# Kernel optimization log

Hardware: AMD Instinct MI355X
Metric: run time of the kernel (lower is better)

Reference implementation:

```python
import jax, jax.numpy as jnp
import numpy as np

N_NODES = 100000
N_EDGES = 1600000
IN_DIM, HID_DIM, LAT_DIM = 128, 128, 32


def setup_inputs() -> dict:
    key = jax.random.key(0)
    k_x, k_e, k_w1, k_w2 = jax.random.split(key, 4)
    x = jax.random.normal(k_x, (N_NODES, IN_DIM), dtype=jnp.float32)
    edge_index = jax.random.randint(k_e, (2, N_EDGES), 0, N_NODES, dtype=jnp.int64)
    # GCNConv weights (glorot-ish scale) and biases
    W1 = jax.random.normal(k_w1, (IN_DIM, HID_DIM), dtype=jnp.float32) / np.sqrt(IN_DIM)
    b1 = jnp.zeros((HID_DIM,), dtype=jnp.float32)
    W2 = jax.random.normal(k_w2, (HID_DIM, LAT_DIM), dtype=jnp.float32) / np.sqrt(HID_DIM)
    b2 = jnp.zeros((LAT_DIM,), dtype=jnp.float32)
    return {"x": x, "edge_index": edge_index, "W1": W1, "b1": b1, "W2": W2, "b2": b2}


def _gcn_layer(x, W, b, src, dst, deg_inv_sqrt, n_nodes):
    # x: [N, Din] -> [N, Dout]; PyG GCNConv: transform, normalize, scatter-add
    xw = x @ W  # [N, Dout]
    norm = deg_inv_sqrt[src] * deg_inv_sqrt[dst]  # [E+N] (self-loops included)
    msg = xw[src] * norm[:, None]  # gather + scale  [E+N, Dout]
    out = jax.ops.segment_sum(msg, dst, num_segments=n_nodes)
    return out + b


def reference(x, edge_index, W1, b1, W2, b2):
    n = x.shape[0]
    loops = jnp.arange(n, dtype=edge_index.dtype)
    # add self-loops (GCNConv default)
    src = jnp.concatenate([edge_index[0], loops])
    dst = jnp.concatenate([edge_index[1], loops])
    # symmetric normalization: deg computed on destination (incl. self-loops)
    deg = jax.ops.segment_sum(jnp.ones_like(dst, dtype=x.dtype), dst, num_segments=n)
    deg_inv_sqrt = jnp.where(deg > 0, jax.lax.rsqrt(deg), 0.0)

    h = _gcn_layer(x, W1, b1, src, dst, deg_inv_sqrt, n)
    h = jax.nn.relu(h)
    # dropout is identity in eval mode
    z = _gcn_layer(h, W2, b2, src, dst, deg_inv_sqrt, n)
    return z
```

## Files before the change

kernel.cpp:

```cpp
#include <hip/hip_runtime.h>


#define KDIM 128
#define PA_NB 196
#define PA_CAP 64
#define PB_CAP 10240

typedef unsigned int uint;
typedef unsigned short ushort;
typedef __attribute__((ext_vector_type(8))) short bf16x8;
typedef __attribute__((ext_vector_type(4))) float f32x4;

__device__ inline ushort f2bf(float f) {
    uint u = __float_as_uint(f);
    return (ushort)((u + 0x7fffu + ((u >> 16) & 1u)) >> 16);
}

__global__ void initw_kernel(int* wcnt, int nwin) {
    int b = threadIdx.x;
    if (b < nwin) wcnt[b] = 0;
}

__global__ __launch_bounds__(256)
void wincount_kernel(const int* __restrict__ dst, int* __restrict__ wcnt, int e, int nwin) {
    __shared__ int lcnt[PA_NB];
    const int tid = threadIdx.x;
    for (int b = tid; b < nwin; b += 256) lcnt[b] = 0;
    __syncthreads();
    int i = blockIdx.x * blockDim.x + tid;
    const int stride = gridDim.x * blockDim.x;
    for (; i < e; i += stride) atomicAdd(&lcnt[dst[i] >> 9], 1);
    __syncthreads();
    for (int b = tid; b < nwin; b += 256) {
        int v = lcnt[b];
        if (v) atomicAdd(&wcnt[b], v);
    }
}

__global__ __launch_bounds__(256)
void winscan_kernel(const int* __restrict__ wcnt, int* __restrict__ winbase,
                    int* __restrict__ gcur, int nwin, int e) {
    __shared__ int ts[256];
    const int t = threadIdx.x;
    int v = (t < nwin) ? wcnt[t] : 0;
    ts[t] = v;
    for (int off = 1; off < 256; off <<= 1) {
        __syncthreads();
        int u = (t >= off) ? ts[t - off] : 0;
        __syncthreads();
        ts[t] += u;
    }
    __syncthreads();
    if (t < nwin) {
        int base = ts[t] - v;
        winbase[t] = base;
        gcur[t] = base;
    }
    if (t == 0) winbase[nwin] = e;
}

__global__ __launch_bounds__(256)
void binA_kernel(const int* __restrict__ src, const int* __restrict__ dst,
                 int* __restrict__ gcur, int* __restrict__ tmp, int e, int nb) {
    __shared__ int lbuf[PA_NB * PA_CAP];
    __shared__ int cnt[PA_NB];
    __shared__ int gbase[PA_NB];
    const int tid = threadIdx.x;
    for (int b = tid; b < nb; b += 256) cnt[b] = 0;
    __syncthreads();

    const int per = (e + gridDim.x - 1) / gridDim.x;
    const int i0 = blockIdx.x * per;
    const int i1 = min(i0 + per, e);
    for (int i = i0 + tid; i < i1; i += 256) {
        int d = dst[i];
        int s = src[i];
        int b = d >> 9;
        int rec = ((d & 511) << 17) | s;
        int p = atomicAdd(&cnt[b], 1);
        if (p < PA_CAP) lbuf[b * PA_CAP + p] = rec;
        else tmp[atomicAdd(&gcur[b], 1)] = rec;
    }
    __syncthreads();
    if (tid < nb) {
        int lvl = min(cnt[tid], PA_CAP);
        cnt[tid] = lvl;
        gbase[tid] = lvl ? atomicAdd(&gcur[tid], lvl) : 0;
    }
    __syncthreads();
    for (int bb = 0; bb < nb; bb += 4) {
        int b = bb + (tid >> 6);
        if (b < nb) {
            int lvl = cnt[b];
            int l = tid & 63;
            if (l < lvl) tmp[gbase[b] + l] = lbuf[b * PA_CAP + l];
        }
    }
}

__global__ __launch_bounds__(256)
void sortB_kernel(const int* __restrict__ tmp, const int* __restrict__ winbase,
                  int* __restrict__ offs, float* __restrict__ dinv,
                  int* __restrict__ csr, int n, int e) {
    __shared__ int lcsr[PB_CAP];
    __shared__ int cnt[512];
    __shared__ int ts[256];
    const int w = blockIdx.x;
    const int tid = threadIdx.x;
    const int node0 = w << 9;
    const int nloc = min(512, n - node0);
    const int base = winbase[w];
    const int end  = winbase[w + 1];

    for (int j = tid; j < 512; j += 256) cnt[j] = 0;
    __syncthreads();
    for (int i = base + tid; i < end; i += 256)
        atomicAdd(&cnt[(tmp[i] >> 17) & 511], 1);
    __syncthreads();

    int a0 = cnt[2 * tid], a1 = cnt[2 * tid + 1];
    int sum = a0 + a1;
    ts[tid] = sum;
    for (int off = 1; off < 256; off <<= 1) {
        __syncthreads();
        int v = (tid >= off) ? ts[tid - off] : 0;
        __syncthreads();
        ts[tid] += v;
    }
    __syncthreads();
    const int ex = ts[tid] - sum;
    if (2 * tid < nloc) {
        offs[node0 + 2 * tid] = base + ex;
        dinv[node0 + 2 * tid] = rsqrtf((float)(a0 + 1));
    }
    if (2 * tid + 1 < nloc) {
        offs[node0 + 2 * tid + 1] = base + ex + a0;
        dinv[node0 + 2 * tid + 1] = rsqrtf((float)(a1 + 1));
    }
    cnt[2 * tid] = ex;
    cnt[2 * tid + 1] = ex + a0;
    if (w == gridDim.x - 1 && tid == 0) offs[n] = e;
    __syncthreads();

    for (int i = base + tid; i < end; i += 256) {
        int rec = tmp[i];
        int dl = (rec >> 17) & 511;
        int s = rec & 0x1FFFF;
        int p = atomicAdd(&cnt[dl], 1);
        if (p < PB_CAP) lcsr[p] = s;
        else csr[base + p] = s;
    }
    __syncthreads();
    const int lim = min(end - base, PB_CAP);
    for (int i = tid; i < lim; i += 256) csr[base + i] = lcsr[i];
}

template<int DOUT>
__global__ void packW_kernel(const float* __restrict__ W, ushort* __restrict__ Wf) {
    int idx = blockIdx.x * blockDim.x + threadIdx.x;
    if (idx >= 128 * DOUT) return;
    int k = idx / DOUT, col = idx % DOUT;
    int c = col >> 4, lcol = col & 15;
    int t = k >> 5, u = (k >> 3) & 3, j = k & 7;
    int lane = u * 16 + lcol;
    Wf[(size_t)(((c * 4 + t) * 64 + lane) * 8 + j)] = f2bf(W[idx]);
}

__global__ __launch_bounds__(256)
void mfma1_kernel(const float* __restrict__ x, const ushort* __restrict__ W1f,
                  const float* __restrict__ dinv, ushort* __restrict__ outb, int n) {
    __shared__ ushort bsm[16384];
    const int tid = threadIdx.x;
    #pragma unroll
    for (int j = 0; j < 8; ++j)
        ((uint4*)bsm)[tid + j * 256] = ((const uint4*)W1f)[tid + j * 256];

    const int w = tid >> 6;
    const int lane = tid & 63;
    const int r = lane & 15;
    const int u = lane >> 4;
    const int row0 = blockIdx.x * 64 + w * 16;
    int arow = row0 + r; if (arow >= n) arow = n - 1;

    bf16x8 afr[4];
    #pragma unroll
    for (int t = 0; t < 4; ++t) {
        const float* px = &x[(size_t)arow * 128 + t * 32 + u * 8];
        f32x4 v0 = *(const f32x4*)px;
        f32x4 v1 = *(const f32x4*)(px + 4);
        bf16x8 a;
        a[0] = (short)f2bf(v0[0]); a[1] = (short)f2bf(v0[1]);
        a[2] = (short)f2bf(v0[2]); a[3] = (short)f2bf(v0[3]);
        a[4] = (short)f2bf(v1[0]); a[5] = (short)f2bf(v1[1]);
        a[6] = (short)f2bf(v1[2]); a[7] = (short)f2bf(v1[3]);
        afr[t] = a;
    }
    __syncthreads();

    f32x4 acc[8];
    #pragma unroll
    for (int c = 0; c < 8; ++c) acc[c] = (f32x4){0.f, 0.f, 0.f, 0.f};

    #pragma unroll
    for (int c = 0; c < 8; ++c) {
        #pragma unroll
        for (int t = 0; t < 4; ++t) {
            bf16x8 b = *(const bf16x8*)&bsm[(size_t)(((c * 4 + t) * 64 + lane) * 8)];
            acc[c] = __builtin_amdgcn_mfma_f32_16x16x32_bf16(afr[t], b, acc[c], 0, 0, 0);
        }
    }

    const int rb = row0 + u * 4;
    f32x4 d4 = *(const f32x4*)&dinv[(rb + 3 < n) ? rb : 0];
    #pragma unroll
    for (int c = 0; c < 8; ++c) {
        #pragma unroll
        for (int rr = 0; rr < 4; ++rr) {
            int row = rb + rr;
            if (row < n) outb[(size_t)row * 128 + c * 16 + r] = f2bf(acc[c][rr] * d4[rr]);
        }
    }
}

__global__ __launch_bounds__(256)
void mfma2_kernel(const ushort* __restrict__ hb, const ushort* __restrict__ W2f,
                  const float* __restrict__ dinv, ushort* __restrict__ outb, int n) {
    __shared__ ushort bsm[4096];
    const int tid = threadIdx.x;
    #pragma unroll
    for (int j = 0; j < 2; ++j)
        ((uint4*)bsm)[tid + j * 256] = ((const uint4*)W2f)[tid + j * 256];

    const int w = tid >> 6;
    const int lane = tid & 63;
    const int r = lane & 15;
    const int u = lane >> 4;
    const int row0 = blockIdx.x * 64 + w * 16;
    int arow = row0 + r; if (arow >= n) arow = n - 1;

    bf16x8 afr[4];
    #pragma unroll
    for (int t = 0; t < 4; ++t)
        afr[t] = *(const bf16x8*)&hb[(size_t)arow * 128 + t * 32 + u * 8];
    __syncthreads();

    f32x4 acc[2];
    acc[0] = (f32x4){0.f, 0.f, 0.f, 0.f};
    acc[1] = (f32x4){0.f, 0.f, 0.f, 0.f};
    #pragma unroll
    for (int c = 0; c < 2; ++c) {
        #pragma unroll
        for (int t = 0; t < 4; ++t) {
            bf16x8 b = *(const bf16x8*)&bsm[(size_t)(((c * 4 + t) * 64 + lane) * 8)];
            acc[c] = __builtin_amdgcn_mfma_f32_16x16x32_bf16(afr[t], b, acc[c], 0, 0, 0);
        }
    }

    const int rb = row0 + u * 4;
    f32x4 d4 = *(const f32x4*)&dinv[(rb + 3 < n) ? rb : 0];
    #pragma unroll
    for (int c = 0; c < 2; ++c) {
        #pragma unroll
        for (int rr = 0; rr < 4; ++rr) {
            int row = rb + rr;
            if (row < n) outb[(size_t)row * 32 + c * 16 + r] = f2bf(acc[c][rr] * d4[rr]);
        }
    }
}

__device__ inline void bf2_add(uint u, float& a0, float& a1) {
    a0 += __uint_as_float(u << 16);
    a1 += __uint_as_float(u & 0xffff0000u);
}

__device__ inline void bf8_add(uint4 u, float* acc) {
    bf2_add(u.x, acc[0], acc[1]);
    bf2_add(u.y, acc[2], acc[3]);
    bf2_add(u.z, acc[4], acc[5]);
    bf2_add(u.w, acc[6], acc[7]);
}

__global__ __launch_bounds__(256)
void agg128_kernel(const ushort* __restrict__ xwb, const int* __restrict__ offs,
                   const int* __restrict__ csr, const float* __restrict__ dinv,
                   const float* __restrict__ bias, ushort* __restrict__ outb, int n) {
    const int w = threadIdx.x >> 6;
    const int i = blockIdx.x * 4 + w;
    if (i >= n) return;
    const int lane = threadIdx.x & 63;
    const int g = lane >> 4;
    const int q = lane & 15;

    float acc[8] = {};
    const int e0 = offs[i], e1 = offs[i + 1];
    int e = e0 + g;
    for (; e + 12 < e1; e += 16) {
        int s0 = csr[e];
        int s1 = csr[e + 4];
        int s2 = csr[e + 8];
        int s3 = csr[e + 12];
        uint4 u0 = *(const uint4*)&xwb[(size_t)s0 * 128 + q * 8];
        uint4 u1 = *(const uint4*)&xwb[(size_t)s1 * 128 + q * 8];
        uint4 u2 = *(const uint4*)&xwb[(size_t)s2 * 128 + q * 8];
        uint4 u3 = *(const uint4*)&xwb[(size_t)s3 * 128 + q * 8];
        bf8_add(u0, acc);
        bf8_add(u1, acc);
        bf8_add(u2, acc);
        bf8_add(u3, acc);
    }
    for (; e < e1; e += 4) {
        int s0 = csr[e];
        uint4 u = *(const uint4*)&xwb[(size_t)s0 * 128 + q * 8];
        bf8_add(u, acc);
    }
    #pragma unroll
    for (int j = 0; j < 8; ++j) {
        acc[j] += __shfl_xor(acc[j], 16, 64);
        acc[j] += __shfl_xor(acc[j], 32, 64);
    }

    if (g == 0) {
        const float di = dinv[i];
        uint4 su = *(const uint4*)&xwb[(size_t)i * 128 + q * 8];
        bf8_add(su, acc);
        const float4 b0 = *(const float4*)&bias[q * 8];
        const float4 b1 = *(const float4*)&bias[q * 8 + 4];
        ushort us[8];
        us[0] = f2bf(fmaxf(acc[0] * di + b0.x, 0.f));
        us[1] = f2bf(fmaxf(acc[1] * di + b0.y, 0.f));
        us[2] = f2bf(fmaxf(acc[2] * di + b0.z, 0.f));
        us[3] = f2bf(fmaxf(acc[3] * di + b0.w, 0.f));
        us[4] = f2bf(fmaxf(acc[4] * di + b1.x, 0.f));
        us[5] = f2bf(fmaxf(acc[5] * di + b1.y, 0.f));
        us[6] = f2bf(fmaxf(acc[6] * di + b1.z, 0.f));
        us[7] = f2bf(fmaxf(acc[7] * di + b1.w, 0.f));
        *(uint4*)&outb[(size_t)i * 128 + q * 8] = *(const uint4*)us;
    }
}

__global__ __launch_bounds__(256)
void agg32_kernel(const ushort* __restrict__ xwb, const int* __restrict__ offs,
                  const int* __restrict__ csr, const float* __restrict__ dinv,
                  const float* __restrict__ bias, float* __restrict__ out, int n) {
    const int w = threadIdx.x >> 6;
    const int i = blockIdx.x * 4 + w;
    if (i >= n) return;
    const int lane = threadIdx.x & 63;
    const int g = lane >> 3;
    const int q = lane & 7;

    float acc[4] = {};
    const int e0 = offs[i], e1 = offs[i + 1];
    int e = e0 + g;
    for (; e + 8 < e1; e += 16) {
        int s0 = csr[e];
        int s1 = csr[e + 8];
        uint2 u0 = *(const uint2*)&xwb[(size_t)s0 * 32 + q * 4];
        uint2 u1 = *(const uint2*)&xwb[(size_t)s1 * 32 + q * 4];
        bf2_add(u0.x, acc[0], acc[1]);
        bf2_add(u0.y, acc[2], acc[3]);
        bf2_add(u1.x, acc[0], acc[1]);
        bf2_add(u1.y, acc[2], acc[3]);
    }
    if (e < e1) {
        int s0 = csr[e];
        uint2 u = *(const uint2*)&xwb[(size_t)s0 * 32 + q * 4];
        bf2_add(u.x, acc[0], acc[1]);
        bf2_add(u.y, acc[2], acc[3]);
    }
    #pragma unroll
    for (int j = 0; j < 4; ++j) {
        acc[j] += __shfl_xor(acc[j], 8, 64);
        acc[j] += __shfl_xor(acc[j], 16, 64);
        acc[j] += __shfl_xor(acc[j], 32, 64);
    }

    if (g == 0) {
        const float di = dinv[i];
        uint2 su = *(const uint2*)&xwb[(size_t)i * 32 + q * 4];
        bf2_add(su.x, acc[0], acc[1]);
        bf2_add(su.y, acc[2], acc[3]);
        const float4 b = *(const float4*)&bias[q * 4];
        float4 r;
        r.x = acc[0] * di + b.x;
        r.y = acc[1] * di + b.y;
        r.z = acc[2] * di + b.z;
        r.w = acc[3] * di + b.w;
        *(float4*)&out[(size_t)i * 32 + q * 4] = r;
    }
}

extern "C" void kernel_launch(void* const* d_in, const int* in_sizes, int n_in,
                              void* d_out, int out_size, void* d_ws, size_t ws_size,
                              hipStream_t stream) {
    const int n = in_sizes[0] / KDIM;
    const int e = in_sizes[1] / 2;

    const float* x  = (const float*)d_in[0];
    const int*   ei = (const int*)d_in[1];
    const int*   src = ei;
    const int*   dst = ei + e;
    const float* W1 = (const float*)d_in[2];
    const float* b1 = (const float*)d_in[3];
    const float* W2 = (const float*)d_in[4];
    const float* b2 = (const float*)d_in[5];
    float* out = (float*)d_out;

    char* p = (char*)d_ws;
    auto alloc = [&](size_t bytes) { char* q = p; p += (bytes + 255) & ~(size_t)255; return q; };
    const int nwin = (n + 511) >> 9;
    float*  dinv    = (float*)alloc((size_t)n * 4);
    int*    offs    = (int*)  alloc((size_t)(n + 1) * 4);
    int*    wcnt    = (int*)  alloc((size_t)nwin * 4);
    int*    winbase = (int*)  alloc((size_t)(nwin + 1) * 4);
    int*    gcur    = (int*)  alloc((size_t)nwin * 4);
    int*    csr     = (int*)  alloc((size_t)e * 4);
    ushort* W1f     = (ushort*)alloc((size_t)128 * 128 * 2);
    ushort* W2f     = (ushort*)alloc((size_t)128 * 32 * 2);
    ushort* xws1    = (ushort*)alloc((size_t)n * 128 * 2);
    ushort* hb      = (ushort*)alloc((size_t)n * 128 * 2);
    ushort* xw2s    = (ushort*)alloc((size_t)n * 32 * 2);
    int*    tmp     = (int*)hb;

    initw_kernel<<<1, 256, 0, stream>>>(wcnt, nwin);
    wincount_kernel<<<1024, 256, 0, stream>>>(dst, wcnt, e, nwin);
    winscan_kernel<<<1, 256, 0, stream>>>(wcnt, winbase, gcur, nwin, e);
    binA_kernel<<<512, 256, 0, stream>>>(src, dst, gcur, tmp, e, nwin);
    sortB_kernel<<<nwin, 256, 0, stream>>>(tmp, winbase, offs, dinv, csr, n, e);
    packW_kernel<128><<<64, 256, 0, stream>>>(W1, W1f);
    packW_kernel<32><<<16, 256, 0, stream>>>(W2, W2f);

    mfma1_kernel<<<(n + 63) / 64, 256, 0, stream>>>(x, W1f, dinv, xws1, n);
    agg128_kernel<<<(n + 3) / 4, 256, 0, stream>>>(xws1, offs, csr, dinv, b1, hb, n);

    mfma2_kernel<<<(n + 63) / 64, 256, 0, stream>>>(hb, W2f, dinv, xw2s, n);
    agg32_kernel<<<(n + 3) / 4, 256, 0, stream>>>(xw2s, offs, csr, dinv, b2, out, n);
}
```

Baseline: 209.1 us.

## Merge weight packing, memset counters, double rows per MFMA block, shrink agg unroll

```diff
diff --git a/kernel.cpp b/kernel.cpp
--- a/kernel.cpp
+++ b/kernel.cpp
@@ -14,11 +14,6 @@
 __device__ inline ushort f2bf(float f) {
     uint u = __float_as_uint(f);
     return (ushort)((u + 0x7fffu + ((u >> 16) & 1u)) >> 16);
-}
-
-__global__ void initw_kernel(int* wcnt, int nwin) {
-    int b = threadIdx.x;
-    if (b < nwin) wcnt[b] = 0;
 }
 
 __global__ __launch_bounds__(256)
@@ -155,15 +150,23 @@
     for (int i = tid; i < lim; i += 256) csr[base + i] = lcsr[i];
 }
 
-template<int DOUT>
-__global__ void packW_kernel(const float* __restrict__ W, ushort* __restrict__ Wf) {
+__global__ void packW_kernel(const float* __restrict__ W1, ushort* __restrict__ W1f,
+                             const float* __restrict__ W2, ushort* __restrict__ W2f) {
     int idx = blockIdx.x * blockDim.x + threadIdx.x;
-    if (idx >= 128 * DOUT) return;
-    int k = idx / DOUT, col = idx % DOUT;
-    int c = col >> 4, lcol = col & 15;
-    int t = k >> 5, u = (k >> 3) & 3, j = k & 7;
-    int lane = u * 16 + lcol;
-    Wf[(size_t)(((c * 4 + t) * 64 + lane) * 8 + j)] = f2bf(W[idx]);
+    if (idx < 16384) {
+        int k = idx >> 7, col = idx & 127;
+        int c = col >> 4, lcol = col & 15;
+        int t = k >> 5, u = (k >> 3) & 3, j = k & 7;
+        int lane = u * 16 + lcol;
+        W1f[(size_t)(((c * 4 + t) * 64 + lane) * 8 + j)] = f2bf(W1[idx]);
+    } else if (idx < 16384 + 4096) {
+        int i2 = idx - 16384;
+        int k = i2 >> 5, col = i2 & 31;
+        int c = col >> 4, lcol = col & 15;
+        int t = k >> 5, u = (k >> 3) & 3, j = k & 7;
+        int lane = u * 16 + lcol;
+        W2f[(size_t)(((c * 4 + t) * 64 + lane) * 8 + j)] = f2bf(W2[i2]);
+    }
 }
 
 __global__ __launch_bounds__(256)
@@ -174,50 +177,52 @@
     #pragma unroll
     for (int j = 0; j < 8; ++j)
         ((uint4*)bsm)[tid + j * 256] = ((const uint4*)W1f)[tid + j * 256];
+    __syncthreads();
 
     const int w = tid >> 6;
     const int lane = tid & 63;
     const int r = lane & 15;
     const int u = lane >> 4;
-    const int row0 = blockIdx.x * 64 + w * 16;
-    int arow = row0 + r; if (arow >= n) arow = n - 1;
-
-    bf16x8 afr[4];
-    #pragma unroll
-    for (int t = 0; t < 4; ++t) {
-        const float* px = &x[(size_t)arow * 128 + t * 32 + u * 8];
-        f32x4 v0 = *(const f32x4*)px;
-        f32x4 v1 = *(const f32x4*)(px + 4);
-        bf16x8 a;
-        a[0] = (short)f2bf(v0[0]); a[1] = (short)f2bf(v0[1]);
-        a[2] = (short)f2bf(v0[2]); a[3] = (short)f2bf(v0[3]);
-        a[4] = (short)f2bf(v1[0]); a[5] = (short)f2bf(v1[1]);
-        a[6] = (short)f2bf(v1[2]); a[7] = (short)f2bf(v1[3]);
-        afr[t] = a;
-    }
-    __syncthreads();
-
-    f32x4 acc[8];
-    #pragma unroll
-    for (int c = 0; c < 8; ++c) acc[c] = (f32x4){0.f, 0.f, 0.f, 0.f};
-
-    #pragma unroll
-    for (int c = 0; c < 8; ++c) {
+
+    for (int rt = 0; rt < 2; ++rt) {
+        const int row0 = blockIdx.x * 128 + rt * 64 + w * 16;
+        int arow = row0 + r; if (arow >= n) arow = n - 1;
+
+        bf16x8 afr[4];
         #pragma unroll
         for (int t = 0; t < 4; ++t) {
-            bf16x8 b = *(const bf16x8*)&bsm[(size_t)(((c * 4 + t) * 64 + lane) * 8)];
-            acc[c] = __builtin_amdgcn_mfma_f32_16x16x32_bf16(afr[t], b, acc[c], 0, 0, 0);
-        }
-    }
-
-    const int rb = row0 + u * 4;
-    f32x4 d4 = *(const f32x4*)&dinv[(rb + 3 < n) ? rb : 0];
-    #pragma unroll
-    for (int c = 0; c < 8; ++c) {
-        #pragma unroll
-        for (int rr = 0; rr < 4; ++rr) {
-            int row = rb + rr;
-            if (row < n) outb[(size_t)row * 128 + c * 16 + r] = f2bf(acc[c][rr] * d4[rr]);
+            const float* px = &x[(size_t)arow * 128 + t * 32 + u * 8];
+            f32x4 v0 = *(const f32x4*)px;
+            f32x4 v1 = *(const f32x4*)(px + 4);
+            bf16x8 a;
+            a[0] = (short)f2bf(v0[0]); a[1] = (short)f2bf(v0[1]);
+            a[2] = (short)f2bf(v0[2]); a[3] = (short)f2bf(v0[3]);
+            a[4] = (short)f2bf(v1[0]); a[5] = (short)f2bf(v1[1]);
+            a[6] = (short)f2bf(v1[2]); a[7] = (short)f2bf(v1[3]);
+            afr[t] = a;
+        }
+
+        f32x4 acc[8];
+        #pragma unroll
+        for (int c = 0; c < 8; ++c) acc[c] = (f32x4){0.f, 0.f, 0.f, 0.f};
+        #pragma unroll
+        for (int c = 0; c < 8; ++c) {
+            #pragma unroll
+            for (int t = 0; t < 4; ++t) {
+                bf16x8 b = *(const bf16x8*)&bsm[(size_t)(((c * 4 + t) * 64 + lane) * 8)];
+                acc[c] = __builtin_amdgcn_mfma_f32_16x16x32_bf16(afr[t], b, acc[c], 0, 0, 0);
+            }
+        }
+
+        const int rb = row0 + u * 4;
+        f32x4 d4 = *(const f32x4*)&dinv[(rb + 3 < n) ? rb : 0];
+        #pragma unroll
+        for (int c = 0; c < 8; ++c) {
+            #pragma unroll
+            for (int rr = 0; rr < 4; ++rr) {
+                int row = rb + rr;
+                if (row < n) outb[(size_t)row * 128 + c * 16 + r] = f2bf(acc[c][rr] * d4[rr]);
+            }
         }
     }
 }
@@ -230,40 +235,43 @@
     #pragma unroll
     for (int j = 0; j < 2; ++j)
         ((uint4*)bsm)[tid + j * 256] = ((const uint4*)W2f)[tid + j * 256];
+    __syncthreads();
 
     const int w = tid >> 6;
     const int lane = tid & 63;
     const int r = lane & 15;
     const int u = lane >> 4;
-    const int row0 = blockIdx.x * 64 + w * 16;
-    int arow = row0 + r; if (arow >= n) arow = n - 1;
-
-    bf16x8 afr[4];
-    #pragma unroll
-    for (int t = 0; t < 4; ++t)
-        afr[t] = *(const bf16x8*)&hb[(size_t)arow * 128 + t * 32 + u * 8];
-    __syncthreads();
-
-    f32x4 acc[2];
-    acc[0] = (f32x4){0.f, 0.f, 0.f, 0.f};
-    acc[1] = (f32x4){0.f, 0.f, 0.f, 0.f};
-    #pragma unroll
-    for (int c = 0; c < 2; ++c) {
-        #pragma unroll
-        for (int t = 0; t < 4; ++t) {
-            bf16x8 b = *(const bf16x8*)&bsm[(size_t)(((c * 4 + t) * 64 + lane) * 8)];
-            acc[c] = __builtin_amdgcn_mfma_f32_16x16x32_bf16(afr[t], b, acc[c], 0, 0, 0);
-        }
-    }
-
-    const int rb = row0 + u * 4;
-    f32x4 d4 = *(const f32x4*)&dinv[(rb + 3 < n) ? rb : 0];
-    #pragma unroll
-    for (int c = 0; c < 2; ++c) {
-        #pragma unroll
-        for (int rr = 0; rr < 4; ++rr) {
-            int row = rb + rr;
-            if (row < n) outb[(size_t)row * 32 + c * 16 + r] = f2bf(acc[c][rr] * d4[rr]);
+
+    for (int rt = 0; rt < 2; ++rt) {
+        const int row0 = blockIdx.x * 128 + rt * 64 + w * 16;
+        int arow = row0 + r; if (arow >= n) arow = n - 1;
+
+        bf16x8 afr[4];
+        #pragma unroll
+        for (int t = 0; t < 4; ++t)
+            afr[t] = *(const bf16x8*)&hb[(size_t)arow * 128 + t * 32 + u * 8];
+
+        f32x4 acc[2];
+        acc[0] = (f32x4){0.f, 0.f, 0.f, 0.f};
+        acc[1] = (f32x4){0.f, 0.f, 0.f, 0.f};
+        #pragma unroll
+        for (int c = 0; c < 2; ++c) {
+            #pragma unroll
+            for (int t = 0; t < 4; ++t) {
+                bf16x8 b = *(const bf16x8*)&bsm[(size_t)(((c * 4 + t) * 64 + lane) * 8)];
+                acc[c] = __builtin_amdgcn_mfma_f32_16x16x32_bf16(afr[t], b, acc[c], 0, 0, 0);
+            }
+        }
+
+        const int rb = row0 + u * 4;
+        f32x4 d4 = *(const f32x4*)&dinv[(rb + 3 < n) ? rb : 0];
+        #pragma unroll
+        for (int c = 0; c < 2; ++c) {
+            #pragma unroll
+            for (int rr = 0; rr < 4; ++rr) {
+                int row = rb + rr;
+                if (row < n) outb[(size_t)row * 32 + c * 16 + r] = f2bf(acc[c][rr] * d4[rr]);
+            }
         }
     }
 }
@@ -294,21 +302,15 @@
     float acc[8] = {};
     const int e0 = offs[i], e1 = offs[i + 1];
     int e = e0 + g;
-    for (; e + 12 < e1; e += 16) {
+    for (; e + 4 < e1; e += 8) {
         int s0 = csr[e];
         int s1 = csr[e + 4];
-        int s2 = csr[e + 8];
-        int s3 = csr[e + 12];
         uint4 u0 = *(const uint4*)&xwb[(size_t)s0 * 128 + q * 8];
         uint4 u1 = *(const uint4*)&xwb[(size_t)s1 * 128 + q * 8];
-        uint4 u2 = *(const uint4*)&xwb[(size_t)s2 * 128 + q * 8];
-        uint4 u3 = *(const uint4*)&xwb[(size_t)s3 * 128 + q * 8];
         bf8_add(u0, acc);
         bf8_add(u1, acc);
-        bf8_add(u2, acc);
-        bf8_add(u3, acc);
-    }
-    for (; e < e1; e += 4) {
+    }
+    if (e < e1) {
         int s0 = csr[e];
         uint4 u = *(const uint4*)&xwb[(size_t)s0 * 128 + q * 8];
         bf8_add(u, acc);
@@ -422,17 +424,16 @@
     ushort* xw2s    = (ushort*)alloc((size_t)n * 32 * 2);
     int*    tmp     = (int*)hb;
 
-    initw_kernel<<<1, 256, 0, stream>>>(wcnt, nwin);
-    wincount_kernel<<<1024, 256, 0, stream>>>(dst, wcnt, e, nwin);
+    hipMemsetAsync(wcnt, 0, (size_t)nwin * 4, stream);
+    wincount_kernel<<<512, 256, 0, stream>>>(dst, wcnt, e, nwin);
     winscan_kernel<<<1, 256, 0, stream>>>(wcnt, winbase, gcur, nwin, e);
-    binA_kernel<<<512, 256, 0, stream>>>(src, dst, gcur, tmp, e, nwin);
+    binA_kernel<<<256, 256, 0, stream>>>(src, dst, gcur, tmp, e, nwin);
     sortB_kernel<<<nwin, 256, 0, stream>>>(tmp, winbase, offs, dinv, csr, n, e);
-    packW_kernel<128><<<64, 256, 0, stream>>>(W1, W1f);
-    packW_kernel<32><<<16, 256, 0, stream>>>(W2, W2f);
-
-    mfma1_kernel<<<(n + 63) / 64, 256, 0, stream>>>(x, W1f, dinv, xws1, n);
+    packW_kernel<<<80, 256, 0, stream>>>(W1, W1f, W2, W2f);
+
+    mfma1_kernel<<<(n + 127) / 128, 256, 0, stream>>>(x, W1f, dinv, xws1, n);
     agg128_kernel<<<(n + 3) / 4, 256, 0, stream>>>(xws1, offs, csr, dinv, b1, hb, n);
 
-    mfma2_kernel<<<(n + 63) / 64, 256, 0, stream>>>(hb, W2f, dinv, xw2s, n);
+    mfma2_kernel<<<(n + 127) / 128, 256, 0, stream>>>(hb, W2f, dinv, xw2s, n);
     agg32_kernel<<<(n + 3) / 4, 256, 0, stream>>>(xw2s, offs, csr, dinv, b2, out, n);
 }
```

Result: faster. 200.5 us (-4.1%).
